# Performance work log

Measured on AMD Instinct MI355X. Metric: run time of the kernel, lower is better.

The kernel has to match this reference:

```python
import jax, jax.numpy as jnp
import numpy as np
from jax import lax

ALPHA = 0.5
GAMMA = 0.01
BIG = 1e8  # stands in for +inf boundary of the soft-DTW DP table


def _softmin3(a, b, c, gamma):
    x = jnp.stack([a, b, c], axis=0)
    return -gamma * jax.nn.logsumexp(-x / gamma, axis=0)


def _softdtw_values(D, gamma):
    """Soft-DTW values for a batch of cost matrices.

    D: [M, N, N] pairwise cost matrices -> [M] soft-DTW values R[N, N].
    Computed with an anti-diagonal lax.scan (2N-1 sequential steps), fully
    vectorized over the batch and over each diagonal.
    """
    M, N, _ = D.shape
    Dpad = jnp.zeros((M, N + 1, N + 1), D.dtype).at[:, 1:, 1:].set(D)
    ii = jnp.arange(N + 1)
    # diagonal d=0: only R[0,0]=0 ; diagonal d=1: R[0,1]=R[1,0]=inf
    prev2 = jnp.full((M, N + 1), BIG, D.dtype).at[:, 0].set(0.0)
    prev1 = jnp.full((M, N + 1), BIG, D.dtype)

    def shift(r):  # r at index i-1, BIG at i=0
        return jnp.concatenate([jnp.full((M, 1), BIG, r.dtype), r[:, :-1]], axis=1)

    def step(carry, d):
        p2, p1 = carry
        j = d - ii
        valid = (ii >= 1) & (ii <= N) & (j >= 1) & (j <= N)
        jc = jnp.clip(j, 0, N)
        dvals = Dpad[:, ii, jc]  # [M, N+1] costs on this diagonal
        # R[i,j] = D[i,j] + softmin(R[i-1,j-1], R[i-1,j], R[i,j-1])
        smin = _softmin3(shift(p2), shift(p1), p1, gamma)
        cur = jnp.where(valid[None, :], dvals + smin, BIG)
        return (p1, cur), None

    (_, cur), _ = lax.scan(step, (prev2, prev1), jnp.arange(2, 2 * N + 1))
    return cur[:, N]  # R[N, N]


def setup_inputs() -> dict:
    key = jax.random.key(0)
    k1, k2 = jax.random.split(key)
    outputs = jax.random.normal(k1, (64, 128, 4), dtype=jnp.float32)
    targets = jax.random.normal(k2, (64, 128, 4), dtype=jnp.float32)
    return {"outputs": outputs, "targets": targets}


def reference(outputs, targets):
    B, T, C = outputs.shape
    # Per (sample, channel): D[i, j] = (target_i - output_j)^2  (rows = target idx)
    t = jnp.transpose(targets, (0, 2, 1)).reshape(B * C, T)
    o = jnp.transpose(outputs, (0, 2, 1)).reshape(B * C, T)
    D = (t[:, :, None] - o[:, None, :]) ** 2  # [B*C, T, T]

    # shape loss: mean over batch of soft-DTW values, summed over channels
    vals = _softdtw_values(D, GAMMA)  # [B*C]
    loss_shape = vals.sum() / B

    # temporal loss: soft alignment path E = d(softDTW)/dD, penalized by (i-j)^2
    path = jax.grad(lambda DD: _softdtw_values(DD, GAMMA).sum())(D)  # [B*C, T, T]
    idx = jnp.arange(1, T + 1, dtype=D.dtype)
    Omega = (idx[:, None] - idx[None, :]) ** 2  # [T, T]
    loss_temporal = (path * Omega).sum() / (B * T * T)

    return ALPHA * loss_shape + (1.0 - ALPHA) * loss_temporal
```

## Files before the change

kernel.cpp:

```cpp
#include <hip/hip_runtime.h>


#define TN 128
#define BATCH 64
#define CH 4

__device__ __forceinline__ float fast_exp2(float x) { return __builtin_amdgcn_exp2f(x); }
__device__ __forceinline__ float fast_log2(float x) { return __builtin_amdgcn_logf(x); }
__device__ __forceinline__ float fast_rcp(float x)  { return __builtin_amdgcn_rcpf(x); }

__device__ __forceinline__ float dpp_shr1(float x, float fill) {
  union { float f; int i; } o, s, r;
  o.f = fill; s.f = x;
  r.i = __builtin_amdgcn_update_dpp(o.i, s.i, 0x138, 0xF, 0xF, false);
  return r.f;
}

__global__ __launch_bounds__(64)
void dilate_softdtw_kernel(const float* __restrict__ outputs,
                           const float* __restrict__ targets,
                           float* __restrict__ out) {
  __shared__ float obuf[384];
  __shared__ float2 Bb[192];

  const float WALLP = -4.328085e6f;
  const float O_PAD = 15.0f;
  const float K2    = 144.2695040888963f;

  const int m = blockIdx.x, b = m >> 2, c = m & 3;
  const int lane = threadIdx.x;

  const float* tb = targets + (size_t)b*(TN*CH) + c;
  const float* ob = outputs + (size_t)b*(TN*CH) + c;

  #pragma unroll
  for (int s = 0; s < 6; ++s) {
    const int idx = lane + 64*s;
    const int k = idx - 126;
    obuf[idx] = ((unsigned)k <= 127u) ? ob[k*CH] : O_PAD;
  }
  const float tA = tb[lane*CH];
  const float tB = tb[(64 + lane)*CH];
  __syncthreads();

  const float* oc = obuf + 126;

  float rRes = 0.f, dRes = 0.f;

  {
    const float t0 = tA;
    float p1  = WALLP;
    float up2 = (lane == 0) ? 0.0f : WALLP;
    float dp1 = 0.f, dup2 = 0.f;
    float fd  = (float)(2*lane);
    float o0  = oc[-lane];

    #pragma unroll 4
    for (int d = 2; d <= 192; ++d) {
      const int j0 = d - 1 - lane;
      const float o_nxt = oc[j0];
      float up1  = dpp_shr1(p1, WALLP);
      float dup1 = dpp_shr1(dp1, 0.f);

      float mn = fmaxf(up2, fmaxf(up1, p1));
      float a = up2 - mn, bq = up1 - mn, cc = p1 - mn;
      float ea = fast_exp2(a);
      float eb = fast_exp2(bq);
      float ec = fast_exp2(cc);
      float sum = (ea + eb) + ec;
      float rs = fast_rcp(sum);
      float l  = fast_log2(sum);
      float df = t0 - o0;
      float q  = df*df;
      float jv = __builtin_fmaf(ea, dup2, __builtin_fmaf(eb, dup1, ec*dp1));
      float w  = fd*fd;
      float cv = __builtin_fmaf(-K2, q, mn + l);
      float dv = __builtin_fmaf(rs, jv, w);

      if (lane == 63) Bb[d - 1] = make_float2(cv, dv);

      up2 = up1; p1 = cv; dup2 = dup1; dp1 = dv;
      o0 = o_nxt; fd -= 1.0f;
    }
  }
  __syncthreads();

  {
    const float t0 = tB;
    float p1  = WALLP, up2 = WALLP;
    float dp1 = 0.f, dup2 = 0.f;
    float fd  = (float)(64 + 2*lane);
    float o0  = oc[-lane];
    float2 bc = Bb[64];

    #pragma unroll 4
    for (int d = 66; d <= 256; ++d) {
      const int j0 = d - 65 - lane;
      const float o_nxt = oc[j0];
      const int bi = (d - 1 > 191) ? 191 : (d - 1);
      const float2 bn = Bb[bi];
      float up1  = dpp_shr1(p1, bc.x);
      float dup1 = dpp_shr1(dp1, bc.y);

      float mn = fmaxf(up2, fmaxf(up1, p1));
      float a = up2 - mn, bq = up1 - mn, cc = p1 - mn;
      float ea = fast_exp2(a);
      float eb = fast_exp2(bq);
      float ec = fast_exp2(cc);
      float sum = (ea + eb) + ec;
      float rs = fast_rcp(sum);
      float l  = fast_log2(sum);
      float df = t0 - o0;
      float q  = df*df;
      float jv = __builtin_fmaf(ea, dup2, __builtin_fmaf(eb, dup1, ec*dp1));
      float w  = fd*fd;
      float cv = __builtin_fmaf(-K2, q, mn + l);
      float dv = __builtin_fmaf(rs, jv, w);

      up2 = up1; p1 = cv; dup2 = dup1; dp1 = dv;
      o0 = o_nxt; fd -= 1.0f; bc = bn;
    }
    rRes = p1; dRes = dp1;
  }

  if (lane == 63) {
    const float partial = __builtin_fmaf(rRes, -5.415212348e-5f,
                                         dRes * 4.76837158203125e-7f);
    atomicAdd(out, partial);
  }
}

extern "C" void kernel_launch(void* const* d_in, const int* in_sizes, int n_in,
                              void* d_out, int out_size, void* d_ws, size_t ws_size,
                              hipStream_t stream) {
  const float* outputs = (const float*)d_in[0];
  const float* targets = (const float*)d_in[1];
  float* out = (float*)d_out;
  (void)in_sizes; (void)n_in; (void)out_size; (void)d_ws; (void)ws_size;

  (void)hipMemsetAsync(out, 0, sizeof(float), stream);
  dilate_softdtw_kernel<<<dim3(256), dim3(64), 0, stream>>>(outputs, targets, out);
}
```

Before: 83.44 us.

## Pipeline the two row-halves across two wavefronts with LDS progress flag

Splits the soft-DTW wavefront sweep so the first 64 rows and the second 64 rows each run on their own wavefront in the same block. Previously one wave ran them back to back. The second wave spins on a shared progress counter that the first wave publishes every 8 diagonals, so the two halves overlap in time. This shortens the sequential critical path, at the cost of spin-wait polling and release/acquire fences in the producer loop.

```diff
diff --git a/kernel.cpp b/kernel.cpp
--- a/kernel.cpp
+++ b/kernel.cpp
@@ -4,6 +4,7 @@
 #define TN 128
 #define BATCH 64
 #define CH 4
+#define KCH 8
 
 __device__ __forceinline__ float fast_exp2(float x) { return __builtin_amdgcn_exp2f(x); }
 __device__ __forceinline__ float fast_log2(float x) { return __builtin_amdgcn_logf(x); }
@@ -16,39 +17,39 @@
   return r.f;
 }
 
-__global__ __launch_bounds__(64)
+__global__ __launch_bounds__(128)
 void dilate_softdtw_kernel(const float* __restrict__ outputs,
                            const float* __restrict__ targets,
                            float* __restrict__ out) {
   __shared__ float obuf[384];
   __shared__ float2 Bb[192];
+  __shared__ int prog;
 
   const float WALLP = -4.328085e6f;
   const float O_PAD = 15.0f;
   const float K2    = 144.2695040888963f;
 
   const int m = blockIdx.x, b = m >> 2, c = m & 3;
-  const int lane = threadIdx.x;
+  const int tid  = threadIdx.x;
+  const int wid  = tid >> 6;
+  const int lane = tid & 63;
 
   const float* tb = targets + (size_t)b*(TN*CH) + c;
   const float* ob = outputs + (size_t)b*(TN*CH) + c;
 
   #pragma unroll
-  for (int s = 0; s < 6; ++s) {
-    const int idx = lane + 64*s;
+  for (int s = 0; s < 3; ++s) {
+    const int idx = tid + 128*s;
     const int k = idx - 126;
     obuf[idx] = ((unsigned)k <= 127u) ? ob[k*CH] : O_PAD;
   }
-  const float tA = tb[lane*CH];
-  const float tB = tb[(64 + lane)*CH];
+  const float t0 = tb[(wid*64 + lane)*CH];
+  if (tid == 0) prog = 0;
   __syncthreads();
 
   const float* oc = obuf + 126;
 
-  float rRes = 0.f, dRes = 0.f;
-
-  {
-    const float t0 = tA;
+  if (wid == 0) {
     float p1  = WALLP;
     float up2 = (lane == 0) ? 0.0f : WALLP;
     float dp1 = 0.f, dup2 = 0.f;
@@ -78,55 +79,65 @@
       float dv = __builtin_fmaf(rs, jv, w);
 
       if (lane == 63) Bb[d - 1] = make_float2(cv, dv);
+      if (((d - 1) & (KCH - 1)) == 0) {
+        if (lane == 63)
+          __hip_atomic_store(&prog, d, __ATOMIC_RELEASE, __HIP_MEMORY_SCOPE_WORKGROUP);
+      }
 
       up2 = up1; p1 = cv; dup2 = dup1; dp1 = dv;
       o0 = o_nxt; fd -= 1.0f;
     }
-  }
-  __syncthreads();
-
-  {
-    const float t0 = tB;
+    if (lane == 63)
+      __hip_atomic_store(&prog, 1000, __ATOMIC_RELEASE, __HIP_MEMORY_SCOPE_WORKGROUP);
+  } else {
     float p1  = WALLP, up2 = WALLP;
     float dp1 = 0.f, dup2 = 0.f;
     float fd  = (float)(64 + 2*lane);
     float o0  = oc[-lane];
-    float2 bc = Bb[64];
+    float2 bc;
+    bool first = true;
 
-    #pragma unroll 4
-    for (int d = 66; d <= 256; ++d) {
-      const int j0 = d - 65 - lane;
-      const float o_nxt = oc[j0];
-      const int bi = (d - 1 > 191) ? 191 : (d - 1);
-      const float2 bn = Bb[bi];
-      float up1  = dpp_shr1(p1, bc.x);
-      float dup1 = dpp_shr1(dp1, bc.y);
+    for (int d0 = 66; d0 <= 256; d0 += KCH) {
+      int target = d0 + KCH - 1;
+      if (target > 185) target = 1000;
+      while (__hip_atomic_load(&prog, __ATOMIC_ACQUIRE, __HIP_MEMORY_SCOPE_WORKGROUP) < target) {}
+      if (first) { bc = Bb[64]; first = false; }
 
-      float mn = fmaxf(up2, fmaxf(up1, p1));
-      float a = up2 - mn, bq = up1 - mn, cc = p1 - mn;
-      float ea = fast_exp2(a);
-      float eb = fast_exp2(bq);
-      float ec = fast_exp2(cc);
-      float sum = (ea + eb) + ec;
-      float rs = fast_rcp(sum);
-      float l  = fast_log2(sum);
-      float df = t0 - o0;
-      float q  = df*df;
-      float jv = __builtin_fmaf(ea, dup2, __builtin_fmaf(eb, dup1, ec*dp1));
-      float w  = fd*fd;
-      float cv = __builtin_fmaf(-K2, q, mn + l);
-      float dv = __builtin_fmaf(rs, jv, w);
+      const int dend = (d0 + KCH - 1 < 256) ? d0 + KCH - 1 : 256;
+      #pragma unroll 4
+      for (int d = d0; d <= dend; ++d) {
+        const int j0 = d - 65 - lane;
+        const float o_nxt = oc[j0];
+        const int bi = (d - 1 > 191) ? 191 : (d - 1);
+        const float2 bn = Bb[bi];
+        float up1  = dpp_shr1(p1, bc.x);
+        float dup1 = dpp_shr1(dp1, bc.y);
 
-      up2 = up1; p1 = cv; dup2 = dup1; dp1 = dv;
-      o0 = o_nxt; fd -= 1.0f; bc = bn;
+        float mn = fmaxf(up2, fmaxf(up1, p1));
+        float a = up2 - mn, bq = up1 - mn, cc = p1 - mn;
+        float ea = fast_exp2(a);
+        float eb = fast_exp2(bq);
+        float ec = fast_exp2(cc);
+        float sum = (ea + eb) + ec;
+        float rs = fast_rcp(sum);
+        float l  = fast_log2(sum);
+        float df = t0 - o0;
+        float q  = df*df;
+        float jv = __builtin_fmaf(ea, dup2, __builtin_fmaf(eb, dup1, ec*dp1));
+        float w  = fd*fd;
+        float cv = __builtin_fmaf(-K2, q, mn + l);
+        float dv = __builtin_fmaf(rs, jv, w);
+
+        up2 = up1; p1 = cv; dup2 = dup1; dp1 = dv;
+        o0 = o_nxt; fd -= 1.0f; bc = bn;
+      }
     }
-    rRes = p1; dRes = dp1;
-  }
 
-  if (lane == 63) {
-    const float partial = __builtin_fmaf(rRes, -5.415212348e-5f,
-                                         dRes * 4.76837158203125e-7f);
-    atomicAdd(out, partial);
+    if (lane == 63) {
+      const float partial = __builtin_fmaf(p1, -5.415212348e-5f,
+                                           dp1 * 4.76837158203125e-7f);
+      atomicAdd(out, partial);
+    }
   }
 }
 
@@ -139,5 +150,5 @@
   (void)in_sizes; (void)n_in; (void)out_size; (void)d_ws; (void)ws_size;
 
   (void)hipMemsetAsync(out, 0, sizeof(float), stream);
-  dilate_softdtw_kernel<<<dim3(256), dim3(64), 0, stream>>>(outputs, targets, out);
+  dilate_softdtw_kernel<<<dim3(256), dim3(128), 0, stream>>>(outputs, targets, out);
 }
```

New measurement: 82.81 us. About the same (-0.7%).
